# Optimization experiments

Hardware: AMD Instinct MI355X
Metric: run time of the kernel (lower is better)

## Reference

```python
import jax, jax.numpy as jnp
import numpy as np

B, N, D, LAT, EC = 1024, 256, 64, 128, 32


def setup_inputs() -> dict:
    key = jax.random.key(0)
    ks = jax.random.split(key, 8)
    s = lambda d: 1.0 / np.sqrt(d)
    return {
        "local_data": jax.random.normal(ks[0], (B, D), jnp.float32),
        "neighbor_data": jax.random.normal(ks[1], (B, N, D), jnp.float32),
        "Wc": jax.random.normal(ks[2], (D, EC), jnp.float32) * s(D),
        "bc": jnp.zeros((EC,), jnp.float32),
        "Wf": jax.random.normal(ks[3], (D, LAT), jnp.float32) * s(D),
        "bf": jnp.zeros((LAT,), jnp.float32),
        "Wa": jax.random.normal(ks[4], (3 * EC, LAT), jnp.float32) * s(3 * EC),
        "ba": jnp.zeros((LAT,), jnp.float32),
        "Wl": jax.random.normal(ks[5], (LAT, LAT), jnp.float32) * s(LAT),
        "bl": jnp.zeros((LAT,), jnp.float32),
    }


def reference(local_data, neighbor_data, Wc, bc, Wf, bf, Wa, ba, Wl, bl):
    # per-neighbor feature encoder: [B,N,LAT]
    enc_feature = jax.nn.relu(jnp.einsum("bnd,dk->bnk", neighbor_data, Wf) + bf)
    # per-neighbor communication encoder: [B,N,EC]
    enc_comm = jax.nn.relu(jnp.einsum("bnd,dk->bnk", neighbor_data, Wc) + bc)
    # self communication embedding: [B,EC]
    enc_comm_self = jax.nn.relu(local_data @ Wc + bc)
    # broadcast self and neighbor-mean to [B,N,EC]
    self_rep = jnp.broadcast_to(enc_comm_self[:, None, :], enc_comm.shape)
    mean_rep = jnp.broadcast_to(enc_comm.mean(axis=1, keepdims=True), enc_comm.shape)
    cat = jnp.concatenate([self_rep, enc_comm, mean_rep], axis=-1)  # [B,N,3*EC]
    # attention: linear then softmax over neighbor axis (dim=-2)
    att = jax.nn.softmax(jnp.einsum("bnc,ck->bnk", cat, Wa) + ba, axis=1)  # [B,N,LAT]
    # attention-weighted sum over neighbors: [B,LAT]
    aggregated = jnp.einsum("bnk,bnk->bk", att, enc_feature)
    # later layer
    return jax.nn.relu(aggregated @ Wl + bl)
```

## Files before the change

### kernel.cpp

```cpp
#include <hip/hip_runtime.h>

#define NB    256
#define DIN   64
#define LATD  128
#define ECD   32

typedef __attribute__((ext_vector_type(8))) __bf16 bf16x8;
typedef __attribute__((ext_vector_type(4))) float f32x4;

#define XS_STRIDE 72
#define EC_STRIDE 40
#define WA_STRIDE 40

#define WS_WC 0
#define WS_WF (32 * 72)
#define WS_WA (32 * 72 + 128 * 72)

#define MFMA(a, b, c) __builtin_amdgcn_mfma_f32_16x16x32_bf16((a), (b), (c), 0, 0, 0)

__device__ __forceinline__ unsigned short f2bf(float f) {
    unsigned u = __builtin_bit_cast(unsigned, f);
    u += 0x7fffu + ((u >> 16) & 1u);
    return (unsigned short)(u >> 16);
}

__device__ __forceinline__ unsigned cvt2(float lo, float hi) {
    unsigned r;
    asm("v_cvt_pk_bf16_f32 %0, %1, %2" : "=v"(r) : "v"(lo), "v"(hi));
    return r;
}

#if __has_builtin(__builtin_amdgcn_exp2f)
__device__ __forceinline__ float fexp2(float x) {
    return __builtin_amdgcn_exp2f(x);
}
#else
__device__ __forceinline__ float fexp2(float x) {
    float r;
    asm("v_exp_f32 %0, %1\n\ts_nop 1" : "=v"(r) : "v"(x));
    return r;
}
#endif

__device__ __forceinline__ bf16x8 pack8(float4 a, float4 b) {
    union { unsigned u[4]; bf16x8 v; } r;
    r.u[0] = cvt2(a.x, a.y);
    r.u[1] = cvt2(a.z, a.w);
    r.u[2] = cvt2(b.x, b.y);
    r.u[3] = cvt2(b.z, b.w);
    return r.v;
}

__global__ __launch_bounds__(256) void prep_kernel(
    const float* __restrict__ Wc, const float* __restrict__ Wf,
    const float* __restrict__ Wa, unsigned short* __restrict__ ws)
{
    int t = blockIdx.x * blockDim.x + threadIdx.x;
    int stride = gridDim.x * blockDim.x;
    for (int i = t; i < 32 * 64; i += stride) {
        int n = i >> 6, k = i & 63;
        ws[WS_WC + n * XS_STRIDE + k] = f2bf(Wc[k * ECD + n]);
    }
    for (int i = t; i < 128 * 64; i += stride) {
        int n = i >> 6, k = i & 63;
        ws[WS_WF + n * XS_STRIDE + k] = f2bf(Wf[k * LATD + n]);
    }
    for (int i = t; i < 128 * 32; i += stride) {
        int n = i >> 5, k = i & 31;
        ws[WS_WA + n * WA_STRIDE + k] = f2bf(Wa[(ECD + k) * LATD + n] * 1.44269504f);
    }
}

__global__ __launch_bounds__(256, 2) void arm_main(
    const float* __restrict__ xg,
    const float* __restrict__ bcv,
    const float* __restrict__ bfv,
    const float* __restrict__ wl,
    const float* __restrict__ blv,
    const unsigned short* __restrict__ ws,
    float* __restrict__ out)
{
    __shared__ unsigned short ecs[NB * EC_STRIDE];
    __shared__ float aggnum[4][LATD];
    __shared__ float aggden[4][LATD];
    __shared__ float aggfull[LATD];
    __shared__ float wlpart[2][LATD];

    const int b0   = blockIdx.x;
    const int b1   = blockIdx.x + 512;
    const int tid  = threadIdx.x;
    const int lane = tid & 63;
    const int w    = tid >> 6;
    const int l15  = lane & 15;
    const int q    = lane >> 4;

    const unsigned short* wfb = ws + WS_WF;
    const unsigned short* wab = ws + WS_WA;

    bf16x8 wfrag[2][2];
    #pragma unroll
    for (int ks = 0; ks < 2; ++ks)
        #pragma unroll
        for (int nb = 0; nb < 2; ++nb)
            wfrag[ks][nb] = *reinterpret_cast<const bf16x8*>(
                &ws[WS_WC + (nb * 16 + l15) * XS_STRIDE + ks * 32 + q * 8]);
    float bc0 = bcv[l15], bc1 = bcv[16 + l15];

    float4 st[4][4];
    {
        const float* xb = xg + (size_t)b0 * NB * DIN;
        #pragma unroll
        for (int t = 0; t < 4; ++t) {
            const float* p = xb + (w * 64 + t * 16 + l15) * DIN + q * 8;
            st[t][0] = *reinterpret_cast<const float4*>(p);
            st[t][1] = *reinterpret_cast<const float4*>(p + 4);
            st[t][2] = *reinterpret_cast<const float4*>(p + 32);
            st[t][3] = *reinterpret_cast<const float4*>(p + 36);
        }
    }

    #pragma unroll
    for (int e = 0; e < 2; ++e) {
        const int b = e ? b1 : b0;

        bf16x8 wf0 = *reinterpret_cast<const bf16x8*>(&wfb[l15 * XS_STRIDE + q * 8]);
        bf16x8 wf1 = *reinterpret_cast<const bf16x8*>(&wfb[l15 * XS_STRIDE + 32 + q * 8]);
        bf16x8 wag = *reinterpret_cast<const bf16x8*>(&wab[l15 * WA_STRIDE + q * 8]);
        float  bfl = bfv[l15];

        bf16x8 xfrag[4][2];
        #pragma unroll
        for (int t = 0; t < 4; ++t) {
            xfrag[t][0] = pack8(st[t][0], st[t][1]);
            xfrag[t][1] = pack8(st[t][2], st[t][3]);
        }

        #pragma unroll
        for (int t = 0; t < 4; ++t) {
            int rowA = w * 64 + t * 16;
            f32x4 a0 = {bc0, bc0, bc0, bc0};
            f32x4 a1 = {bc1, bc1, bc1, bc1};
            #pragma unroll
            for (int ks = 0; ks < 2; ++ks) {
                a0 = MFMA(xfrag[t][ks], wfrag[ks][0], a0);
                a1 = MFMA(xfrag[t][ks], wfrag[ks][1], a1);
            }
            #pragma unroll
            for (int r = 0; r < 4; ++r) {
                int row = rowA + q * 4 + r;
                unsigned pk = cvt2(fmaxf(a0[r], 0.f), fmaxf(a1[r], 0.f));
                ecs[row * EC_STRIDE + l15]      = (unsigned short)pk;
                ecs[row * EC_STRIDE + 16 + l15] = (unsigned short)(pk >> 16);
            }
        }

        bf16x8 ecfrag[4];
        #pragma unroll
        for (int t = 0; t < 4; ++t)
            ecfrag[t] = *reinterpret_cast<const bf16x8*>(
                &ecs[(w * 64 + t * 16 + l15) * EC_STRIDE + q * 8]);

        if (e == 0) {
            const float* xb = xg + (size_t)b1 * NB * DIN;
            #pragma unroll
            for (int t = 0; t < 4; ++t) {
                const float* p = xb + (w * 64 + t * 16 + l15) * DIN + q * 8;
                st[t][0] = *reinterpret_cast<const float4*>(p);
                st[t][1] = *reinterpret_cast<const float4*>(p + 4);
                st[t][2] = *reinterpret_cast<const float4*>(p + 32);
                st[t][3] = *reinterpret_cast<const float4*>(p + 36);
            }
        }

        for (int g = 0; g < 8; ++g) {
            bf16x8 nwf0, nwf1, nwag;
            float  nbfl = 0.f;
            if (g < 7) {
                int r0 = (g + 1) * 16 + l15;
                nwf0 = *reinterpret_cast<const bf16x8*>(&wfb[r0 * XS_STRIDE + q * 8]);
                nwf1 = *reinterpret_cast<const bf16x8*>(&wfb[r0 * XS_STRIDE + 32 + q * 8]);
                nwag = *reinterpret_cast<const bf16x8*>(&wab[r0 * WA_STRIDE + q * 8]);
                nbfl = bfv[r0];
            }

            float num = 0.f, den = 0.f;
            #pragma unroll
            for (int t = 0; t < 4; ++t) {
                f32x4 z = {bfl, bfl, bfl, bfl};
                z = MFMA(xfrag[t][0], wf0, z);
                f32x4 ef = MFMA(xfrag[t][1], wf1, z);
                f32x4 z2 = {0.f, 0.f, 0.f, 0.f};
                f32x4 lg = MFMA(ecfrag[t], wag, z2);
                #pragma unroll
                for (int r = 0; r < 4; ++r) {
                    float e2 = fmaxf(ef[r], 0.f);
                    float p  = fexp2(lg[r]);
                    num = fmaf(p, e2, num);
                    den += p;
                }
            }
            num += __shfl_xor(num, 16, 64); num += __shfl_xor(num, 32, 64);
            den += __shfl_xor(den, 16, 64); den += __shfl_xor(den, 32, 64);
            if (lane < 16) {
                aggnum[w][g * 16 + lane] = num;
                aggden[w][g * 16 + lane] = den;
            }

            if (g < 7) { wf0 = nwf0; wf1 = nwf1; wag = nwag; bfl = nbfl; }
        }
        __syncthreads();

        if (tid < 128) {
            float num = aggnum[0][tid] + aggnum[1][tid] + aggnum[2][tid] + aggnum[3][tid];
            float den = aggden[0][tid] + aggden[1][tid] + aggden[2][tid] + aggden[3][tid];
            aggfull[tid] = num / den;
        }
        __syncthreads();

        {
            int c = tid & 127, h = tid >> 7;
            float acc = 0.f;
            #pragma unroll 16
            for (int k = h * 64; k < h * 64 + 64; ++k)
                acc += aggfull[k] * wl[k * LATD + c];
            wlpart[h][c] = acc;
        }
        __syncthreads();
        if (tid < 128)
            out[(size_t)b * LATD + tid] =
                fmaxf(wlpart[0][tid] + wlpart[1][tid] + blv[tid], 0.f);
    }
}

extern "C" void kernel_launch(void* const* d_in, const int* in_sizes, int n_in,
                              void* d_out, int out_size, void* d_ws, size_t ws_size,
                              hipStream_t stream)
{
    const float* xg  = (const float*)d_in[1];
    const float* wc  = (const float*)d_in[2];
    const float* bc_ = (const float*)d_in[3];
    const float* wf  = (const float*)d_in[4];
    const float* bf_ = (const float*)d_in[5];
    const float* wa  = (const float*)d_in[6];
    const float* wl  = (const float*)d_in[8];
    const float* bl_ = (const float*)d_in[9];
    unsigned short* wsp = (unsigned short*)d_ws;
    float* out = (float*)d_out;

    prep_kernel<<<8, 256, 0, stream>>>(wc, wf, wa, wsp);
    arm_main<<<512, 256, 0, stream>>>(xg, bc_, bf_, wl, bl_, wsp, out);
}
```

Measured before the change: 125.9 us.

## Process both batch elements together in the attention and output loops

Both batch items are now loaded up front and converted to bf16, their comm encodings are computed, and then a single 8-group loop runs the feature, attention MFMAs and softmax accumulation for both items. Each weight fragment load from the workspace is therefore shared by two items, and the final Wl projection reads each Wl value once for both outputs. This also halves the number of block barriers and keeps all 256 threads busy in the reduction and output stages. The cost is higher register pressure: two sets of x fragments and ecs fragments stay live, which could spill or lower occupancy under launch_bounds(256,2). Loading the second item's input is also no longer overlapped with compute on the first.

```diff
diff --git a/kernel.cpp b/kernel.cpp
--- a/kernel.cpp
+++ b/kernel.cpp
@@ -81,10 +81,10 @@
     float* __restrict__ out)
 {
     __shared__ unsigned short ecs[NB * EC_STRIDE];
-    __shared__ float aggnum[4][LATD];
-    __shared__ float aggden[4][LATD];
-    __shared__ float aggfull[LATD];
-    __shared__ float wlpart[2][LATD];
+    __shared__ float aggnum[2][4][LATD];
+    __shared__ float aggden[2][4][LATD];
+    __shared__ float aggfull[2][LATD];
+    __shared__ float wlpart[2][2][LATD];
 
     const int b0   = blockIdx.x;
     const int b1   = blockIdx.x + 512;
@@ -106,35 +106,43 @@
                 &ws[WS_WC + (nb * 16 + l15) * XS_STRIDE + ks * 32 + q * 8]);
     float bc0 = bcv[l15], bc1 = bcv[16 + l15];
 
-    float4 st[4][4];
-    {
-        const float* xb = xg + (size_t)b0 * NB * DIN;
-        #pragma unroll
-        for (int t = 0; t < 4; ++t) {
-            const float* p = xb + (w * 64 + t * 16 + l15) * DIN + q * 8;
-            st[t][0] = *reinterpret_cast<const float4*>(p);
-            st[t][1] = *reinterpret_cast<const float4*>(p + 4);
-            st[t][2] = *reinterpret_cast<const float4*>(p + 32);
-            st[t][3] = *reinterpret_cast<const float4*>(p + 36);
-        }
-    }
-
+    float4 st0[4][4], st1[4][4];
+    {
+        const float* xa = xg + (size_t)b0 * NB * DIN;
+        const float* xc = xg + (size_t)b1 * NB * DIN;
+        #pragma unroll
+        for (int t = 0; t < 4; ++t) {
+            const float* p = xa + (w * 64 + t * 16 + l15) * DIN + q * 8;
+            st0[t][0] = *reinterpret_cast<const float4*>(p);
+            st0[t][1] = *reinterpret_cast<const float4*>(p + 4);
+            st0[t][2] = *reinterpret_cast<const float4*>(p + 32);
+            st0[t][3] = *reinterpret_cast<const float4*>(p + 36);
+        }
+        #pragma unroll
+        for (int t = 0; t < 4; ++t) {
+            const float* p = xc + (w * 64 + t * 16 + l15) * DIN + q * 8;
+            st1[t][0] = *reinterpret_cast<const float4*>(p);
+            st1[t][1] = *reinterpret_cast<const float4*>(p + 4);
+            st1[t][2] = *reinterpret_cast<const float4*>(p + 32);
+            st1[t][3] = *reinterpret_cast<const float4*>(p + 36);
+        }
+    }
+
+    bf16x8 xfrag[2][4][2];
+    #pragma unroll
+    for (int t = 0; t < 4; ++t) {
+        xfrag[0][t][0] = pack8(st0[t][0], st0[t][1]);
+        xfrag[0][t][1] = pack8(st0[t][2], st0[t][3]);
+    }
+    #pragma unroll
+    for (int t = 0; t < 4; ++t) {
+        xfrag[1][t][0] = pack8(st1[t][0], st1[t][1]);
+        xfrag[1][t][1] = pack8(st1[t][2], st1[t][3]);
+    }
+
+    bf16x8 ecfrag[2][4];
     #pragma unroll
     for (int e = 0; e < 2; ++e) {
-        const int b = e ? b1 : b0;
-
-        bf16x8 wf0 = *reinterpret_cast<const bf16x8*>(&wfb[l15 * XS_STRIDE + q * 8]);
-        bf16x8 wf1 = *reinterpret_cast<const bf16x8*>(&wfb[l15 * XS_STRIDE + 32 + q * 8]);
-        bf16x8 wag = *reinterpret_cast<const bf16x8*>(&wab[l15 * WA_STRIDE + q * 8]);
-        float  bfl = bfv[l15];
-
-        bf16x8 xfrag[4][2];
-        #pragma unroll
-        for (int t = 0; t < 4; ++t) {
-            xfrag[t][0] = pack8(st[t][0], st[t][1]);
-            xfrag[t][1] = pack8(st[t][2], st[t][3]);
-        }
-
         #pragma unroll
         for (int t = 0; t < 4; ++t) {
             int rowA = w * 64 + t * 16;
@@ -142,8 +150,8 @@
             f32x4 a1 = {bc1, bc1, bc1, bc1};
             #pragma unroll
             for (int ks = 0; ks < 2; ++ks) {
-                a0 = MFMA(xfrag[t][ks], wfrag[ks][0], a0);
-                a1 = MFMA(xfrag[t][ks], wfrag[ks][1], a1);
+                a0 = MFMA(xfrag[e][t][ks], wfrag[ks][0], a0);
+                a1 = MFMA(xfrag[e][t][ks], wfrag[ks][1], a1);
             }
             #pragma unroll
             for (int r = 0; r < 4; ++r) {
@@ -153,82 +161,93 @@
                 ecs[row * EC_STRIDE + 16 + l15] = (unsigned short)(pk >> 16);
             }
         }
-
-        bf16x8 ecfrag[4];
         #pragma unroll
         for (int t = 0; t < 4; ++t)
-            ecfrag[t] = *reinterpret_cast<const bf16x8*>(
+            ecfrag[e][t] = *reinterpret_cast<const bf16x8*>(
                 &ecs[(w * 64 + t * 16 + l15) * EC_STRIDE + q * 8]);
-
-        if (e == 0) {
-            const float* xb = xg + (size_t)b1 * NB * DIN;
+    }
+
+    bf16x8 wf0 = *reinterpret_cast<const bf16x8*>(&wfb[l15 * XS_STRIDE + q * 8]);
+    bf16x8 wf1 = *reinterpret_cast<const bf16x8*>(&wfb[l15 * XS_STRIDE + 32 + q * 8]);
+    bf16x8 wag = *reinterpret_cast<const bf16x8*>(&wab[l15 * WA_STRIDE + q * 8]);
+    float  bfl = bfv[l15];
+
+    for (int g = 0; g < 8; ++g) {
+        bf16x8 nwf0, nwf1, nwag;
+        float  nbfl = 0.f;
+        if (g < 7) {
+            int r0 = (g + 1) * 16 + l15;
+            nwf0 = *reinterpret_cast<const bf16x8*>(&wfb[r0 * XS_STRIDE + q * 8]);
+            nwf1 = *reinterpret_cast<const bf16x8*>(&wfb[r0 * XS_STRIDE + 32 + q * 8]);
+            nwag = *reinterpret_cast<const bf16x8*>(&wab[r0 * WA_STRIDE + q * 8]);
+            nbfl = bfv[r0];
+        }
+
+        float num0 = 0.f, den0 = 0.f, num1 = 0.f, den1 = 0.f;
+        #pragma unroll
+        for (int t = 0; t < 4; ++t) {
+            f32x4 za = {bfl, bfl, bfl, bfl};
+            za = MFMA(xfrag[0][t][0], wf0, za);
+            f32x4 efa = MFMA(xfrag[0][t][1], wf1, za);
+            f32x4 zz0 = {0.f, 0.f, 0.f, 0.f};
+            f32x4 lga = MFMA(ecfrag[0][t], wag, zz0);
+            f32x4 zb = {bfl, bfl, bfl, bfl};
+            zb = MFMA(xfrag[1][t][0], wf0, zb);
+            f32x4 efb = MFMA(xfrag[1][t][1], wf1, zb);
+            f32x4 zz1 = {0.f, 0.f, 0.f, 0.f};
+            f32x4 lgb = MFMA(ecfrag[1][t], wag, zz1);
             #pragma unroll
-            for (int t = 0; t < 4; ++t) {
-                const float* p = xb + (w * 64 + t * 16 + l15) * DIN + q * 8;
-                st[t][0] = *reinterpret_cast<const float4*>(p);
-                st[t][1] = *reinterpret_cast<const float4*>(p + 4);
-                st[t][2] = *reinterpret_cast<const float4*>(p + 32);
-                st[t][3] = *reinterpret_cast<const float4*>(p + 36);
+            for (int r = 0; r < 4; ++r) {
+                float ea = fmaxf(efa[r], 0.f);
+                float pa = fexp2(lga[r]);
+                num0 = fmaf(pa, ea, num0);
+                den0 += pa;
+                float eb = fmaxf(efb[r], 0.f);
+                float pb = fexp2(lgb[r]);
+                num1 = fmaf(pb, eb, num1);
+                den1 += pb;
             }
         }
-
-        for (int g = 0; g < 8; ++g) {
-            bf16x8 nwf0, nwf1, nwag;
-            float  nbfl = 0.f;
-            if (g < 7) {
-                int r0 = (g + 1) * 16 + l15;
-                nwf0 = *reinterpret_cast<const bf16x8*>(&wfb[r0 * XS_STRIDE + q * 8]);
-                nwf1 = *reinterpret_cast<const bf16x8*>(&wfb[r0 * XS_STRIDE + 32 + q * 8]);
-                nwag = *reinterpret_cast<const bf16x8*>(&wab[r0 * WA_STRIDE + q * 8]);
-                nbfl = bfv[r0];
-            }
-
-            float num = 0.f, den = 0.f;
-            #pragma unroll
-            for (int t = 0; t < 4; ++t) {
-                f32x4 z = {bfl, bfl, bfl, bfl};
-                z = MFMA(xfrag[t][0], wf0, z);
-                f32x4 ef = MFMA(xfrag[t][1], wf1, z);
-                f32x4 z2 = {0.f, 0.f, 0.f, 0.f};
-                f32x4 lg = MFMA(ecfrag[t], wag, z2);
-                #pragma unroll
-                for (int r = 0; r < 4; ++r) {
-                    float e2 = fmaxf(ef[r], 0.f);
-                    float p  = fexp2(lg[r]);
-                    num = fmaf(p, e2, num);
-                    den += p;
-                }
-            }
-            num += __shfl_xor(num, 16, 64); num += __shfl_xor(num, 32, 64);
-            den += __shfl_xor(den, 16, 64); den += __shfl_xor(den, 32, 64);
-            if (lane < 16) {
-                aggnum[w][g * 16 + lane] = num;
-                aggden[w][g * 16 + lane] = den;
-            }
-
-            if (g < 7) { wf0 = nwf0; wf1 = nwf1; wag = nwag; bfl = nbfl; }
-        }
-        __syncthreads();
-
-        if (tid < 128) {
-            float num = aggnum[0][tid] + aggnum[1][tid] + aggnum[2][tid] + aggnum[3][tid];
-            float den = aggden[0][tid] + aggden[1][tid] + aggden[2][tid] + aggden[3][tid];
-            aggfull[tid] = num / den;
-        }
-        __syncthreads();
-
-        {
-            int c = tid & 127, h = tid >> 7;
-            float acc = 0.f;
-            #pragma unroll 16
-            for (int k = h * 64; k < h * 64 + 64; ++k)
-                acc += aggfull[k] * wl[k * LATD + c];
-            wlpart[h][c] = acc;
-        }
-        __syncthreads();
-        if (tid < 128)
-            out[(size_t)b * LATD + tid] =
-                fmaxf(wlpart[0][tid] + wlpart[1][tid] + blv[tid], 0.f);
+        num0 += __shfl_xor(num0, 16, 64); num0 += __shfl_xor(num0, 32, 64);
+        den0 += __shfl_xor(den0, 16, 64); den0 += __shfl_xor(den0, 32, 64);
+        num1 += __shfl_xor(num1, 16, 64); num1 += __shfl_xor(num1, 32, 64);
+        den1 += __shfl_xor(den1, 16, 64); den1 += __shfl_xor(den1, 32, 64);
+        if (lane < 16) {
+            aggnum[0][w][g * 16 + lane] = num0;
+            aggden[0][w][g * 16 + lane] = den0;
+            aggnum[1][w][g * 16 + lane] = num1;
+            aggden[1][w][g * 16 + lane] = den1;
+        }
+
+        if (g < 7) { wf0 = nwf0; wf1 = nwf1; wag = nwag; bfl = nbfl; }
+    }
+    __syncthreads();
+
+    {
+        int e = tid >> 7, c = tid & 127;
+        float num = aggnum[e][0][c] + aggnum[e][1][c] + aggnum[e][2][c] + aggnum[e][3][c];
+        float den = aggden[e][0][c] + aggden[e][1][c] + aggden[e][2][c] + aggden[e][3][c];
+        aggfull[e][c] = num / den;
+    }
+    __syncthreads();
+
+    {
+        int c = tid & 127, h = tid >> 7;
+        float acc0 = 0.f, acc1 = 0.f;
+        #pragma unroll 16
+        for (int k = h * 64; k < h * 64 + 64; ++k) {
+            float wv = wl[k * LATD + c];
+            acc0 = fmaf(aggfull[0][k], wv, acc0);
+            acc1 = fmaf(aggfull[1][k], wv, acc1);
+        }
+        wlpart[h][0][c] = acc0;
+        wlpart[h][1][c] = acc1;
+    }
+    __syncthreads();
+    {
+        int e = tid >> 7, c = tid & 127;
+        out[(size_t)(e ? b1 : b0) * LATD + c] =
+            fmaxf(wlpart[0][e][c] + wlpart[1][e][c] + blv[c], 0.f);
     }
 }
 
```

After: 124.7 us. About the same (-1.0%).
